# Kernel tuning notes

Measured on AMD Instinct MI355X. Metric: run time of the kernel, lower is better.

## Reference

```python
import jax, jax.numpy as jnp
import numpy as np

PACE = 1.0  # regulate_len pace argument (default)


def setup_inputs() -> dict:
    key = jax.random.key(0)
    k1, k2 = jax.random.split(key)
    B, T, D = 16, 512, 384
    MEL_MAX_LEN = 2048
    durations = jax.random.randint(k1, (B, T), 0, 8).astype(jnp.int64)
    enc_out = jax.random.normal(k2, (B, T, D), dtype=jnp.float32)
    return {"durations": durations, "enc_out": enc_out, "mel_max_len": MEL_MAX_LEN}


def reference(durations, enc_out, mel_max_len):
    """Faithful jax port of FastPitch regulate_len (duration-based length
    regulation via indicator-matrix matmul), with the mel_max_len cap applied
    by constructing the frame range directly at the capped length (equivalent
    to building at max_len then slicing [:, :mel_max_len])."""
    dtype = enc_out.dtype
    # reps = int(dur / pace + 0.5)  (truncation == floor for nonneg values)
    reps = jnp.floor(durations.astype(jnp.float32) / PACE + 0.5).astype(jnp.int32)  # [B, T]
    dec_lens = jnp.sum(reps, axis=1)  # [B]
    # cumulative frame boundaries, padded with leading 0: [B, T+1]
    reps_cumsum = jnp.cumsum(jnp.pad(reps, ((0, 0), (1, 0))), axis=1).astype(dtype)
    # frame index range: [1, L, 1]
    range_ = jnp.arange(mel_max_len, dtype=dtype)[None, :, None]
    # indicator: frame l belongs to token t iff cumsum[t] <= l < cumsum[t+1]
    starts = reps_cumsum[:, None, :-1]  # [B, 1, T]
    ends = reps_cumsum[:, None, 1:]     # [B, 1, T]
    mult = ((starts <= range_) & (ends > range_)).astype(dtype)  # [B, L, T]
    # gather-by-matmul: [B, L, T] @ [B, T, D] -> [B, L, D]
    enc_rep = jnp.einsum('blt,btd->bld', mult, enc_out)
    dec_lens = jnp.minimum(dec_lens, mel_max_len)
    return enc_rep, dec_lens
```

## Files before the change

### kernel.cpp

```cpp
#include <hip/hip_runtime.h>

#define NB 16
#define NT 512
#define ND 384
#define MEL 2048
#define PACE 1.0f

__global__ __launch_bounds__(NT) void fp_build_map(const int* __restrict__ durations,
                                                   int* __restrict__ idxmap,
                                                   float* __restrict__ dec_out) {
    const int b = blockIdx.x;
    const int t = threadIdx.x;
    __shared__ int s[NT];

    for (int l = t; l < MEL; l += NT) idxmap[b * MEL + l] = -1;

    const int d = durations[b * NT + t];
    const int rep = (int)floorf((float)d / PACE + 0.5f);
    s[t] = rep;
    __syncthreads();

    for (int off = 1; off < NT; off <<= 1) {
        int tmp = (t >= off) ? s[t - off] : 0;
        __syncthreads();
        s[t] += tmp;
        __syncthreads();
    }

    const int end = s[t];
    const int start = end - rep;
    for (int l = start; l < end && l < MEL; ++l) {
        idxmap[b * MEL + l] = t;
    }

    if (t == NT - 1) {
        int total = s[NT - 1];
        if (total > MEL) total = MEL;
        dec_out[b] = (float)total;
    }
}

__global__ __launch_bounds__(256) void fp_gather(const float4* __restrict__ enc4,
                                                 const int* __restrict__ idxmap,
                                                 float4* __restrict__ out4) {
    const int V = ND / 4;
    const int total = NB * MEL * V;
    const int stride = gridDim.x * blockDim.x;
    for (int f = blockIdx.x * blockDim.x + threadIdx.x; f < total; f += stride) {
        const int row = f / V;
        const int v = f - row * V;
        const int t = idxmap[row];
        float4 r = make_float4(0.f, 0.f, 0.f, 0.f);
        if (t >= 0) {
            const int b = row / MEL;
            r = enc4[(b * NT + t) * V + v];
        }
        out4[f] = r;
    }
}

extern "C" void kernel_launch(void* const* d_in, const int* in_sizes, int n_in,
                              void* d_out, int out_size, void* d_ws, size_t ws_size,
                              hipStream_t stream) {
    const int* durations = (const int*)d_in[0];
    const float* enc_out = (const float*)d_in[1];

    float* out = (float*)d_out;
    float* dec_out = out + (size_t)NB * MEL * ND;
    int* idxmap = (int*)d_ws;

    fp_build_map<<<NB, NT, 0, stream>>>(durations, idxmap, dec_out);

    const int threads = 256;
    const int blocks = 2048;
    fp_gather<<<blocks, threads, 0, stream>>>((const float4*)enc_out, idxmap,
                                              (float4*)out);
}
```

Before: 87.27 us.

## Fuse index-map build and gather into one kernel using per-chunk binary search

```diff
diff --git a/kernel.cpp b/kernel.cpp
--- a/kernel.cpp
+++ b/kernel.cpp
@@ -4,58 +4,63 @@
 #define NT 512
 #define ND 384
 #define MEL 2048
+#define FPB 128
+#define CPB (MEL / FPB)
+#define V4 (ND / 4)
 #define PACE 1.0f
 
-__global__ __launch_bounds__(NT) void fp_build_map(const int* __restrict__ durations,
-                                                   int* __restrict__ idxmap,
+__global__ __launch_bounds__(512) void fp_regulate(const int* __restrict__ durations,
+                                                   const float4* __restrict__ enc4,
+                                                   float4* __restrict__ out4,
                                                    float* __restrict__ dec_out) {
-    const int b = blockIdx.x;
-    const int t = threadIdx.x;
-    __shared__ int s[NT];
+    const int b = blockIdx.x / CPB;
+    const int chunk = blockIdx.x % CPB;
+    const int tid = threadIdx.x;
 
-    for (int l = t; l < MEL; l += NT) idxmap[b * MEL + l] = -1;
+    __shared__ int cum[NT];
+    __shared__ int tok[FPB];
 
-    const int d = durations[b * NT + t];
+    const int d = durations[b * NT + tid];
     const int rep = (int)floorf((float)d / PACE + 0.5f);
-    s[t] = rep;
+    cum[tid] = rep;
+    __syncthreads();
+    for (int off = 1; off < NT; off <<= 1) {
+        const int tmp = (tid >= off) ? cum[tid - off] : 0;
+        __syncthreads();
+        cum[tid] += tmp;
+        __syncthreads();
+    }
+    const int total = cum[NT - 1];
+
+    if (chunk == 0 && tid == 0) {
+        dec_out[b] = (float)(total < MEL ? total : MEL);
+    }
+
+    const int l0 = chunk * FPB;
+    if (tid < FPB) {
+        const int l = l0 + tid;
+        int t = -1;
+        if (l < total) {
+            int lo = 0, hi = NT - 1;
+            while (lo < hi) {
+                const int mid = (lo + hi) >> 1;
+                if (cum[mid] > l) hi = mid; else lo = mid + 1;
+            }
+            t = lo;
+        }
+        tok[tid] = t;
+    }
     __syncthreads();
 
-    for (int off = 1; off < NT; off <<= 1) {
-        int tmp = (t >= off) ? s[t - off] : 0;
-        __syncthreads();
-        s[t] += tmp;
-        __syncthreads();
-    }
-
-    const int end = s[t];
-    const int start = end - rep;
-    for (int l = start; l < end && l < MEL; ++l) {
-        idxmap[b * MEL + l] = t;
-    }
-
-    if (t == NT - 1) {
-        int total = s[NT - 1];
-        if (total > MEL) total = MEL;
-        dec_out[b] = (float)total;
-    }
-}
-
-__global__ __launch_bounds__(256) void fp_gather(const float4* __restrict__ enc4,
-                                                 const int* __restrict__ idxmap,
-                                                 float4* __restrict__ out4) {
-    const int V = ND / 4;
-    const int total = NB * MEL * V;
-    const int stride = gridDim.x * blockDim.x;
-    for (int f = blockIdx.x * blockDim.x + threadIdx.x; f < total; f += stride) {
-        const int row = f / V;
-        const int v = f - row * V;
-        const int t = idxmap[row];
-        float4 r = make_float4(0.f, 0.f, 0.f, 0.f);
-        if (t >= 0) {
-            const int b = row / MEL;
-            r = enc4[(b * NT + t) * V + v];
-        }
-        out4[f] = r;
+    const float4 zero = make_float4(0.f, 0.f, 0.f, 0.f);
+    float4* __restrict__ dst = out4 + (size_t)(b * MEL + l0) * V4;
+    const float4* __restrict__ src_b = enc4 + (size_t)b * NT * V4;
+    #pragma unroll
+    for (int e = tid; e < FPB * V4; e += 512) {
+        const int f = e / V4;
+        const int v = e - f * V4;
+        const int t = tok[f];
+        dst[e] = (t >= 0) ? src_b[(size_t)t * V4 + v] : zero;
     }
 }
 
@@ -67,12 +72,7 @@
 
     float* out = (float*)d_out;
     float* dec_out = out + (size_t)NB * MEL * ND;
-    int* idxmap = (int*)d_ws;
 
-    fp_build_map<<<NB, NT, 0, stream>>>(durations, idxmap, dec_out);
-
-    const int threads = 256;
-    const int blocks = 2048;
-    fp_gather<<<blocks, threads, 0, stream>>>((const float4*)enc_out, idxmap,
-                                              (float4*)out);
+    fp_regulate<<<NB * CPB, 512, 0, stream>>>(durations, (const float4*)enc_out,
+                                              (float4*)out, dec_out);
 }
```

Result: no change. 87.42 us (+0.2%).
